# Performance work log

Measured on AMD Instinct MI355X. Metric: run time of the kernel, lower is better.

Reference implementation:

```python
import jax, jax.numpy as jnp
import numpy as np

N_NODES = 100000
N_EDGES = 1600000
NFEAT = 512
HIDDEN = 128
NCLASS = 40


def setup_inputs() -> dict:
    key = jax.random.key(0)
    ks = jax.random.split(key, 8)
    x = jax.random.normal(ks[0], (N_NODES, NFEAT), dtype=jnp.float32)
    edge_src = jax.random.randint(ks[1], (N_EDGES,), 0, N_NODES, dtype=jnp.int32)
    edge_dst = jax.random.randint(ks[2], (N_EDGES,), 0, N_NODES, dtype=jnp.int32)
    # normalized adjacency values (D^-1/2 A D^-1/2 style), all positive
    edge_val = jax.random.uniform(ks[3], (N_EDGES,), dtype=jnp.float32)
    # glorot-ish init like pygcn's reset_parameters
    W1 = jax.random.normal(ks[4], (NFEAT, HIDDEN), dtype=jnp.float32) / np.sqrt(NFEAT)
    b1 = jnp.zeros((HIDDEN,), dtype=jnp.float32)
    W2 = jax.random.normal(ks[5], (HIDDEN, NCLASS), dtype=jnp.float32) / np.sqrt(HIDDEN)
    b2 = jnp.zeros((NCLASS,), dtype=jnp.float32)
    return {"x": x, "edge_src": edge_src, "edge_dst": edge_dst, "edge_val": edge_val,
            "W1": W1, "b1": b1, "W2": W2, "b2": b2}


def _gcn_layer(h, edge_src, edge_dst, edge_val, W, b):
    # support = h @ W ; out = spmm(adj, support) + b
    support = h @ W                                  # [N, d_out]
    msg = support[edge_src] * edge_val[:, None]      # [E, d_out] gather
    agg = jax.ops.segment_sum(msg, edge_dst, num_segments=N_NODES)  # scatter-add
    return agg + b


def reference(x, edge_src, edge_dst, edge_val, W1, b1, W2, b2):
    h = _gcn_layer(x, edge_src, edge_dst, edge_val, W1, b1)
    h = jax.nn.relu(h)
    # dropout=0.0 -> branch skipped (faithful to `if self.dropout:` with falsy value)
    h = _gcn_layer(h, edge_src, edge_dst, edge_val, W2, b2)
    return jax.nn.log_softmax(h, axis=1)
```

## Files before the change

kernel.cpp:

```cpp
#include <hip/hip_runtime.h>
#include <stdint.h>

#define NN 100000
#define NE 1600000
#define NF 512
#define NH 128
#define NC 40
#define NGB 782

typedef float f32x4 __attribute__((ext_vector_type(4)));
typedef short bf16x8 __attribute__((ext_vector_type(8)));

__device__ __forceinline__ unsigned short f2bf(float f){
    unsigned u = __float_as_uint(f);
    u = u + 0x7FFFu + ((u >> 16) & 1u);
    return (unsigned short)(u >> 16);
}
__device__ __forceinline__ unsigned pk2(float a, float b){
    return (unsigned)f2bf(a) | ((unsigned)f2bf(b) << 16);
}
__device__ __forceinline__ float blo(unsigned u){ return __uint_as_float(u << 16); }
__device__ __forceinline__ float bhi(unsigned u){ return __uint_as_float(u & 0xffff0000u); }
__device__ __forceinline__ float pval(unsigned p){ return __uint_as_float((p & 0x7fffu) << 16); }
__device__ __forceinline__ unsigned psrc(unsigned p){ return p >> 15; }

__global__ __launch_bounds__(256) void wprep(const float* __restrict__ W1, const float* __restrict__ W2,
                                             unsigned short* __restrict__ W1t, unsigned short* __restrict__ W2t){
    int tid = blockIdx.x * 256 + threadIdx.x;
    if (tid < NF * NH){
        int c = tid >> 9;
        int k = tid & 511;
        W1t[c * NF + k] = f2bf(W1[k * NH + c]);
    }
    int t2 = tid - NF * NH;
    if (t2 >= 0 && t2 < 48 * NH){
        int c = t2 >> 7;
        int k = t2 & 127;
        W2t[c * NH + k] = (c < NC) ? f2bf(W2[k * NC + c]) : (unsigned short)0;
    }
}

__global__ __launch_bounds__(256, 3) void gemm1_edge(const float* __restrict__ x,
                                                     const unsigned short* __restrict__ W1t,
                                                     unsigned short* __restrict__ s1,
                                                     const int* __restrict__ esrc,
                                                     const int* __restrict__ edst,
                                                     const float* __restrict__ eval,
                                                     unsigned* __restrict__ pkc){
    __shared__ unsigned short Al[2][128 * 40];
    __shared__ unsigned short Bl[2][128 * 40];
    if (blockIdx.x >= NGB){
        int tid = (blockIdx.x - NGB) * 256 + threadIdx.x;
        if (tid < NE){
            int d = edst[tid];
            unsigned pv = ((unsigned)esrc[tid] << 15) | ((unsigned)f2bf(eval[tid]) & 0x7fffu);
            unsigned pos = atomicAdd(&pkc[(size_t)d * 64], 1u);
            if (pos < 63u)
                pkc[(size_t)d * 64 + 1 + pos] = pv;
        }
        return;
    }
    const int tid  = threadIdx.x;
    const int wid  = tid >> 6;
    const int lane = tid & 63;
    const int quad = lane >> 4;
    const int l15  = lane & 15;
    const int br   = blockIdx.x * 128;

    const int r    = tid >> 1;
    const int half = tid & 1;

    int arow = br + r; if (arow >= NN) arow = NN - 1;
    const float* aptr = x + (size_t)arow * NF + half * 16;
    const unsigned short* bptr = W1t + (size_t)r * NF + half * 16;

    float4 pa0, pa1, pa2, pa3;
    uint4  pb0, pb1;
    {
        const float4* ap = (const float4*)aptr;
        pa0 = ap[0]; pa1 = ap[1]; pa2 = ap[2]; pa3 = ap[3];
        const uint4* bp = (const uint4*)bptr;
        pb0 = bp[0]; pb1 = bp[1];
        unsigned* Ad = (unsigned*)&Al[0][r * 40 + half * 16];
        Ad[0] = pk2(pa0.x, pa0.y); Ad[1] = pk2(pa0.z, pa0.w);
        Ad[2] = pk2(pa1.x, pa1.y); Ad[3] = pk2(pa1.z, pa1.w);
        Ad[4] = pk2(pa2.x, pa2.y); Ad[5] = pk2(pa2.z, pa2.w);
        Ad[6] = pk2(pa3.x, pa3.y); Ad[7] = pk2(pa3.z, pa3.w);
        uint4* Bd = (uint4*)&Bl[0][r * 40 + half * 16];
        Bd[0] = pb0; Bd[1] = pb1;
    }
    __syncthreads();

    f32x4 acc[2][8];
#pragma unroll
    for (int i = 0; i < 2; i++)
#pragma unroll
        for (int j = 0; j < 8; j++) acc[i][j] = (f32x4){0.f, 0.f, 0.f, 0.f};

    int cur = 0;
    for (int ks = 0; ks < NF; ks += 32){
        const bool more = (ks + 32 < NF);
        if (more){
            const float4* ap = (const float4*)(aptr + ks + 32);
            pa0 = ap[0]; pa1 = ap[1]; pa2 = ap[2]; pa3 = ap[3];
            const uint4* bp = (const uint4*)(bptr + ks + 32);
            pb0 = bp[0]; pb1 = bp[1];
        }

        bf16x8 a0 = *(const bf16x8*)&Al[cur][(wid * 32 +      l15) * 40 + quad * 8];
        bf16x8 a1 = *(const bf16x8*)&Al[cur][(wid * 32 + 16 + l15) * 40 + quad * 8];
        bf16x8 bb[8];
#pragma unroll
        for (int ct = 0; ct < 8; ct++)
            bb[ct] = *(const bf16x8*)&Bl[cur][(ct * 16 + l15) * 40 + quad * 8];
#pragma unroll
        for (int ct = 0; ct < 8; ct++){
            acc[0][ct] = __builtin_amdgcn_mfma_f32_16x16x32_bf16(a0, bb[ct], acc[0][ct], 0, 0, 0);
            acc[1][ct] = __builtin_amdgcn_mfma_f32_16x16x32_bf16(a1, bb[ct], acc[1][ct], 0, 0, 0);
        }

        if (more){
            int nxt = cur ^ 1;
            unsigned* Ad = (unsigned*)&Al[nxt][r * 40 + half * 16];
            Ad[0] = pk2(pa0.x, pa0.y); Ad[1] = pk2(pa0.z, pa0.w);
            Ad[2] = pk2(pa1.x, pa1.y); Ad[3] = pk2(pa1.z, pa1.w);
            Ad[4] = pk2(pa2.x, pa2.y); Ad[5] = pk2(pa2.z, pa2.w);
            Ad[6] = pk2(pa3.x, pa3.y); Ad[7] = pk2(pa3.z, pa3.w);
            uint4* Bd = (uint4*)&Bl[nxt][r * 40 + half * 16];
            Bd[0] = pb0; Bd[1] = pb1;
        }
        __syncthreads();
        cur ^= 1;
    }

#pragma unroll
    for (int rt = 0; rt < 2; rt++)
#pragma unroll
        for (int ct = 0; ct < 8; ct++)
#pragma unroll
            for (int i = 0; i < 4; i++){
                int row = br + wid * 32 + rt * 16 + quad * 4 + i;
                if (row < NN) s1[(size_t)row * NH + ct * 16 + l15] = f2bf(acc[rt][ct][i]);
            }
}

__global__ __launch_bounds__(256) void agg1g2(const uint4* __restrict__ s1v,
                                              const unsigned* __restrict__ pkc,
                                              const float* __restrict__ b1,
                                              const unsigned short* __restrict__ W2t,
                                              unsigned short* __restrict__ s2p){
    __shared__ unsigned short Hl[64][136];
    const int tid   = threadIdx.x;
    const int wid   = tid >> 6;
    const int lane  = tid & 63;
    const int quad  = lane >> 4;
    const int hl    = lane & 15;
    const int lbase = quad * 16;
    const int nb    = blockIdx.x * 64;

    const float4* b1v = (const float4*)b1;
    const float4 bA = b1v[2 * hl], bB = b1v[2 * hl + 1];

#pragma unroll
    for (int pass = 0; pass < 4; pass++){
        const int nloc = pass * 16 + wid * 4 + quad;
        const int node = nb + nloc;
        float a[8];
#pragma unroll
        for (int t = 0; t < 8; t++) a[t] = 0.f;

        if (node < NN){
            const unsigned sbase = (unsigned)node * 64;
            unsigned rec = pkc[sbase + hl];
            unsigned cntw = __shfl(rec, lbase, 64);
            int dg = (cntw > 63u) ? 63 : (int)cntw;
            int done = 0, lskip = 1;
            unsigned sb = sbase;
            while (done < dg){
                int cnt = dg - done;
                int room = 16 - lskip; if (cnt > room) cnt = room;
                unsigned curc = rec;
                unsigned nsb = sb + 16;
                if (done + cnt < dg) rec = pkc[nsb + hl];
                int j = 0;
                for (; j + 8 <= cnt; j += 8){
                    unsigned ps[8];
#pragma unroll
                    for (int q = 0; q < 8; q++) ps[q] = __shfl(curc, lbase + lskip + j + q, 64);
                    uint4 us[8];
#pragma unroll
                    for (int q = 0; q < 8; q++) us[q] = s1v[(size_t)psrc(ps[q]) * 16 + hl];
#pragma unroll
                    for (int q = 0; q < 8; q++){
                        float v = pval(ps[q]);
                        a[0] += v * blo(us[q].x); a[1] += v * bhi(us[q].x);
                        a[2] += v * blo(us[q].y); a[3] += v * bhi(us[q].y);
                        a[4] += v * blo(us[q].z); a[5] += v * bhi(us[q].z);
                        a[6] += v * blo(us[q].w); a[7] += v * bhi(us[q].w);
                    }
                }
                for (; j + 4 <= cnt; j += 4){
                    unsigned ps[4];
#pragma unroll
                    for (int q = 0; q < 4; q++) ps[q] = __shfl(curc, lbase + lskip + j + q, 64);
                    uint4 us[4];
#pragma unroll
                    for (int q = 0; q < 4; q++) us[q] = s1v[(size_t)psrc(ps[q]) * 16 + hl];
#pragma unroll
                    for (int q = 0; q < 4; q++){
                        float v = pval(ps[q]);
                        a[0] += v * blo(us[q].x); a[1] += v * bhi(us[q].x);
                        a[2] += v * blo(us[q].y); a[3] += v * bhi(us[q].y);
                        a[4] += v * blo(us[q].z); a[5] += v * bhi(us[q].z);
                        a[6] += v * blo(us[q].w); a[7] += v * bhi(us[q].w);
                    }
                }
                for (; j < cnt; j++){
                    unsigned p = __shfl(curc, lbase + lskip + j, 64);
                    float v = pval(p);
                    uint4 u  = s1v[(size_t)psrc(p) * 16 + hl];
                    a[0] += v * blo(u.x); a[1] += v * bhi(u.x);
                    a[2] += v * blo(u.y); a[3] += v * bhi(u.y);
                    a[4] += v * blo(u.z); a[5] += v * bhi(u.z);
                    a[6] += v * blo(u.w); a[7] += v * bhi(u.w);
                }
                done += cnt; sb = nsb; lskip = 0;
            }
            a[0] += bA.x; a[1] += bA.y; a[2] += bA.z; a[3] += bA.w;
            a[4] += bB.x; a[5] += bB.y; a[6] += bB.z; a[7] += bB.w;
#pragma unroll
            for (int t = 0; t < 8; t++) a[t] = fmaxf(a[t], 0.f);
        }
        *(uint4*)&Hl[nloc][hl * 8] = make_uint4(pk2(a[0], a[1]), pk2(a[2], a[3]),
                                                pk2(a[4], a[5]), pk2(a[6], a[7]));
    }
    __syncthreads();

    bf16x8 bf[3][4];
#pragma unroll
    for (int ct = 0; ct < 3; ct++)
#pragma unroll
        for (int ks = 0; ks < 4; ks++)
            bf[ct][ks] = *(const bf16x8*)&W2t[(ct * 16 + hl) * NH + ks * 32 + quad * 8];

    bf16x8 af[4];
#pragma unroll
    for (int ks = 0; ks < 4; ks++)
        af[ks] = *(const bf16x8*)&Hl[wid * 16 + hl][ks * 32 + quad * 8];

    f32x4 acc[3];
#pragma unroll
    for (int ct = 0; ct < 3; ct++) acc[ct] = (f32x4){0.f, 0.f, 0.f, 0.f};
#pragma unroll
    for (int ks = 0; ks < 4; ks++)
#pragma unroll
        for (int ct = 0; ct < 3; ct++)
            acc[ct] = __builtin_amdgcn_mfma_f32_16x16x32_bf16(af[ks], bf[ct][ks], acc[ct], 0, 0, 0);

#pragma unroll
    for (int ct = 0; ct < 3; ct++)
#pragma unroll
        for (int i = 0; i < 4; i++){
            int row = nb + wid * 16 + quad * 4 + i;
            if (row < NN) s2p[(size_t)row * 64 + ct * 16 + hl] = f2bf(acc[ct][i]);
        }
}

__global__ __launch_bounds__(256) void agg2(const uint4* __restrict__ s2v,
                                            const unsigned* __restrict__ pkc,
                                            const float* __restrict__ b2, float* __restrict__ out){
    const int lane  = threadIdx.x & 63;
    const int oct   = lane >> 3;
    const int hl    = lane & 7;
    const int lbase = oct * 8;
    const int node  = blockIdx.x * 32 + (threadIdx.x >> 6) * 8 + oct;

    float a[8];
#pragma unroll
    for (int t = 0; t < 8; t++) a[t] = 0.f;

    const unsigned sbase = (unsigned)node * 64;
    unsigned rec = pkc[sbase + hl];
    unsigned cntw = __shfl(rec, lbase, 64);
    int dg = (cntw > 63u) ? 63 : (int)cntw;
    int done = 0, lskip = 1;
    unsigned sb = sbase;
    while (done < dg){
        int cnt = dg - done;
        int room = 8 - lskip; if (cnt > room) cnt = room;
        unsigned curc = rec;
        unsigned nsb = sb + 8;
        if (done + cnt < dg) rec = pkc[nsb + hl];
        int j = 0;
        for (; j + 4 <= cnt; j += 4){
            unsigned ps[4];
#pragma unroll
            for (int q = 0; q < 4; q++) ps[q] = __shfl(curc, lbase + lskip + j + q, 64);
            uint4 us[4];
#pragma unroll
            for (int q = 0; q < 4; q++) us[q] = s2v[(size_t)psrc(ps[q]) * 8 + hl];
#pragma unroll
            for (int q = 0; q < 4; q++){
                float v = pval(ps[q]);
                a[0] += v * blo(us[q].x); a[1] += v * bhi(us[q].x);
                a[2] += v * blo(us[q].y); a[3] += v * bhi(us[q].y);
                a[4] += v * blo(us[q].z); a[5] += v * bhi(us[q].z);
                a[6] += v * blo(us[q].w); a[7] += v * bhi(us[q].w);
            }
        }
        for (; j < cnt; j++){
            unsigned p = __shfl(curc, lbase + lskip + j, 64);
            float v = pval(p);
            uint4 u  = s2v[(size_t)psrc(p) * 8 + hl];
            a[0] += v * blo(u.x); a[1] += v * bhi(u.x);
            a[2] += v * blo(u.y); a[3] += v * bhi(u.y);
            a[4] += v * blo(u.z); a[5] += v * bhi(u.z);
            a[6] += v * blo(u.w); a[7] += v * bhi(u.w);
        }
        done += cnt; sb = nsb; lskip = 0;
    }
    const bool act = hl < 5;
    float z[8];
    if (act){
        const float4* b2v = (const float4*)b2;
        float4 cA = b2v[2 * hl], cB = b2v[2 * hl + 1];
        z[0] = a[0] + cA.x; z[1] = a[1] + cA.y; z[2] = a[2] + cA.z; z[3] = a[3] + cA.w;
        z[4] = a[4] + cB.x; z[5] = a[5] + cB.y; z[6] = a[6] + cB.z; z[7] = a[7] + cB.w;
    } else {
#pragma unroll
        for (int t = 0; t < 8; t++) z[t] = -INFINITY;
    }
    float m = z[0];
#pragma unroll
    for (int t = 1; t < 8; t++) m = fmaxf(m, z[t]);
#pragma unroll
    for (int o = 4; o; o >>= 1) m = fmaxf(m, __shfl_xor(m, o, 64));
    float pe = 0.f;
    if (act){
#pragma unroll
        for (int t = 0; t < 8; t++) pe += __expf(z[t] - m);
    }
#pragma unroll
    for (int o = 4; o; o >>= 1) pe += __shfl_xor(pe, o, 64);
    if (act){
        float l = __logf(pe) + m;
        float* op = out + (size_t)node * NC + 8 * hl;
        *(float4*)op       = make_float4(z[0] - l, z[1] - l, z[2] - l, z[3] - l);
        *(float4*)(op + 4) = make_float4(z[4] - l, z[5] - l, z[6] - l, z[7] - l);
    }
}

extern "C" void kernel_launch(void* const* d_in, const int* in_sizes, int n_in,
                              void* d_out, int out_size, void* d_ws, size_t ws_size,
                              hipStream_t stream) {
    const float* x    = (const float*)d_in[0];
    const int*   esrc = (const int*)  d_in[1];
    const int*   edst = (const int*)  d_in[2];
    const float* eval = (const float*)d_in[3];
    const float* W1   = (const float*)d_in[4];
    const float* b1   = (const float*)d_in[5];
    const float* W2   = (const float*)d_in[6];
    const float* b2   = (const float*)d_in[7];
    float* out = (float*)d_out;

    char* ws = (char*)d_ws;
    size_t off = 0;
    auto alloc = [&](size_t bytes) -> void* {
        void* p = ws + off;
        off += (bytes + 255) & ~(size_t)255;
        return p;
    };
    unsigned short* W1t  = (unsigned short*)alloc((size_t)NF * NH * 2);
    unsigned short* W2t  = (unsigned short*)alloc((size_t)48 * NH * 2);
    unsigned short* s1   = (unsigned short*)alloc((size_t)NN * NH * 2);
    unsigned short* s2p  = (unsigned short*)alloc((size_t)NN * 64 * 2);
    unsigned*       pkc  = (unsigned*)     alloc((size_t)NN * 64 * 4);

    hipMemsetAsync(pkc, 0, (size_t)NN * 64 * 4, stream);

    wprep     <<<280, 256, 0, stream>>>(W1, W2, W1t, W2t);
    gemm1_edge<<<NGB + (NE + 255) / 256, 256, 0, stream>>>(x, W1t, s1, esrc, edst, eval, pkc);
    agg1g2    <<<(NN + 63) / 64, 256, 0, stream>>>((const uint4*)s1, pkc, b1, W2t, s2p);
    agg2      <<<NN / 32, 256, 0, stream>>>((const uint4*)s2p, pkc, b2, out);
}
```

Baseline: 511.7 us.

## Split degree counters from edge slots and fold edge binning into GEMM blocks

Moves the per-node degree counter out of the packed edge-slot array into a separate padded array, so only that small array is memset instead of the whole 25.6MB slot buffer. Edge binning is now spread over the GEMM blocks: each block loads 8 edges per thread and does the atomics before the GEMM, then writes the packed records after it. This hides the atomic latency behind the matrix work and drops the extra edge-only blocks. The aggregation kernels read the degree from the new array and no longer skip a header slot, and the middle 4-wide unroll path is removed. Costs are extra registers held across the GEMM, which may lower occupancy, and each GEMM block must now cover 2048 edges.

```diff
diff --git a/kernel.cpp b/kernel.cpp
--- a/kernel.cpp
+++ b/kernel.cpp
@@ -6,7 +6,9 @@
 #define NF 512
 #define NH 128
 #define NC 40
+#define DEGS 16
 #define NGB 782
+#define EPB 2048
 
 typedef float f32x4 __attribute__((ext_vector_type(4)));
 typedef short bf16x8 __attribute__((ext_vector_type(8)));
@@ -46,21 +48,28 @@
                                                      const int* __restrict__ esrc,
                                                      const int* __restrict__ edst,
                                                      const float* __restrict__ eval,
+                                                     unsigned* __restrict__ deg,
                                                      unsigned* __restrict__ pkc){
     __shared__ unsigned short Al[2][128 * 40];
     __shared__ unsigned short Bl[2][128 * 40];
-    if (blockIdx.x >= NGB){
-        int tid = (blockIdx.x - NGB) * 256 + threadIdx.x;
-        if (tid < NE){
-            int d = edst[tid];
-            unsigned pv = ((unsigned)esrc[tid] << 15) | ((unsigned)f2bf(eval[tid]) & 0x7fffu);
-            unsigned pos = atomicAdd(&pkc[(size_t)d * 64], 1u);
-            if (pos < 63u)
-                pkc[(size_t)d * 64 + 1 + pos] = pv;
-        }
-        return;
-    }
     const int tid  = threadIdx.x;
+
+    unsigned epv[8]; unsigned epos[8]; int edd[8];
+    {
+        const int ebase = blockIdx.x * EPB + tid;
+#pragma unroll
+        for (int i = 0; i < 8; i++){
+            int e = ebase + i * 256;
+            bool ok = e < NE;
+            int d      = ok ? edst[e] : 0;
+            int sv     = ok ? esrc[e] : 0;
+            float ev   = ok ? eval[e] : 0.f;
+            edd[i] = d;
+            epv[i] = ((unsigned)sv << 15) | ((unsigned)f2bf(ev) & 0x7fffu);
+            epos[i] = ok ? atomicAdd(&deg[d * DEGS], 1u) : 64u;
+        }
+    }
+
     const int wid  = tid >> 6;
     const int lane = tid & 63;
     const int quad = lane >> 4;
@@ -142,9 +151,16 @@
                 int row = br + wid * 32 + rt * 16 + quad * 4 + i;
                 if (row < NN) s1[(size_t)row * NH + ct * 16 + l15] = f2bf(acc[rt][ct][i]);
             }
+
+#pragma unroll
+    for (int i = 0; i < 8; i++){
+        if (epos[i] < 64u)
+            pkc[(size_t)edd[i] * 64 + epos[i]] = epv[i];
+    }
 }
 
 __global__ __launch_bounds__(256) void agg1g2(const uint4* __restrict__ s1v,
+                                              const unsigned* __restrict__ deg,
                                               const unsigned* __restrict__ pkc,
                                               const float* __restrict__ b1,
                                               const unsigned short* __restrict__ W2t,
@@ -170,23 +186,26 @@
         for (int t = 0; t < 8; t++) a[t] = 0.f;
 
         if (node < NN){
-            const unsigned sbase = (unsigned)node * 64;
-            unsigned rec = pkc[sbase + hl];
-            unsigned cntw = __shfl(rec, lbase, 64);
-            int dg = (cntw > 63u) ? 63 : (int)cntw;
-            int done = 0, lskip = 1;
-            unsigned sb = sbase;
-            while (done < dg){
-                int cnt = dg - done;
-                int room = 16 - lskip; if (cnt > room) cnt = room;
+            const unsigned s = (unsigned)node * 64;
+            unsigned dgv = deg[node * DEGS]; int dg = (dgv > 64u) ? 64 : (int)dgv;
+            const unsigned e = s + dg;
+
+            unsigned rec = 0;
+            { int c0 = dg > 16 ? 16 : dg; if (hl < c0) rec = pkc[s + hl]; }
+            for (unsigned base = s; base < e; base += 16){
+                int cnt = (int)(e - base); if (cnt > 16) cnt = 16;
                 unsigned curc = rec;
-                unsigned nsb = sb + 16;
-                if (done + cnt < dg) rec = pkc[nsb + hl];
+                unsigned nxb = base + 16;
+                if (nxb < e){
+                    int cn = (int)(e - nxb); if (cn > 16) cn = 16;
+                    rec = 0;
+                    if (hl < cn) rec = pkc[nxb + hl];
+                }
                 int j = 0;
                 for (; j + 8 <= cnt; j += 8){
                     unsigned ps[8];
 #pragma unroll
-                    for (int q = 0; q < 8; q++) ps[q] = __shfl(curc, lbase + lskip + j + q, 64);
+                    for (int q = 0; q < 8; q++) ps[q] = __shfl(curc, lbase + j + q, 64);
                     uint4 us[8];
 #pragma unroll
                     for (int q = 0; q < 8; q++) us[q] = s1v[(size_t)psrc(ps[q]) * 16 + hl];
@@ -199,24 +218,8 @@
                         a[6] += v * blo(us[q].w); a[7] += v * bhi(us[q].w);
                     }
                 }
-                for (; j + 4 <= cnt; j += 4){
-                    unsigned ps[4];
-#pragma unroll
-                    for (int q = 0; q < 4; q++) ps[q] = __shfl(curc, lbase + lskip + j + q, 64);
-                    uint4 us[4];
-#pragma unroll
-                    for (int q = 0; q < 4; q++) us[q] = s1v[(size_t)psrc(ps[q]) * 16 + hl];
-#pragma unroll
-                    for (int q = 0; q < 4; q++){
-                        float v = pval(ps[q]);
-                        a[0] += v * blo(us[q].x); a[1] += v * bhi(us[q].x);
-                        a[2] += v * blo(us[q].y); a[3] += v * bhi(us[q].y);
-                        a[4] += v * blo(us[q].z); a[5] += v * bhi(us[q].z);
-                        a[6] += v * blo(us[q].w); a[7] += v * bhi(us[q].w);
-                    }
-                }
                 for (; j < cnt; j++){
-                    unsigned p = __shfl(curc, lbase + lskip + j, 64);
+                    unsigned p = __shfl(curc, lbase + j, 64);
                     float v = pval(p);
                     uint4 u  = s1v[(size_t)psrc(p) * 16 + hl];
                     a[0] += v * blo(u.x); a[1] += v * bhi(u.x);
@@ -224,7 +227,6 @@
                     a[4] += v * blo(u.z); a[5] += v * bhi(u.z);
                     a[6] += v * blo(u.w); a[7] += v * bhi(u.w);
                 }
-                done += cnt; sb = nsb; lskip = 0;
             }
             a[0] += bA.x; a[1] += bA.y; a[2] += bA.z; a[3] += bA.w;
             a[4] += bB.x; a[5] += bB.y; a[6] += bB.z; a[7] += bB.w;
@@ -267,6 +269,7 @@
 }
 
 __global__ __launch_bounds__(256) void agg2(const uint4* __restrict__ s2v,
+                                            const unsigned* __restrict__ deg,
                                             const unsigned* __restrict__ pkc,
                                             const float* __restrict__ b2, float* __restrict__ out){
     const int lane  = threadIdx.x & 63;
@@ -279,23 +282,26 @@
 #pragma unroll
     for (int t = 0; t < 8; t++) a[t] = 0.f;
 
-    const unsigned sbase = (unsigned)node * 64;
-    unsigned rec = pkc[sbase + hl];
-    unsigned cntw = __shfl(rec, lbase, 64);
-    int dg = (cntw > 63u) ? 63 : (int)cntw;
-    int done = 0, lskip = 1;
-    unsigned sb = sbase;
-    while (done < dg){
-        int cnt = dg - done;
-        int room = 8 - lskip; if (cnt > room) cnt = room;
+    const unsigned s = (unsigned)node * 64;
+    unsigned dgv = deg[node * DEGS]; int dg = (dgv > 64u) ? 64 : (int)dgv;
+    const unsigned e = s + dg;
+
+    unsigned rec = 0;
+    { int c0 = dg > 8 ? 8 : dg; if (hl < c0) rec = pkc[s + hl]; }
+    for (unsigned base = s; base < e; base += 8){
+        int cnt = (int)(e - base); if (cnt > 8) cnt = 8;
         unsigned curc = rec;
-        unsigned nsb = sb + 8;
-        if (done + cnt < dg) rec = pkc[nsb + hl];
+        unsigned nxb = base + 8;
+        if (nxb < e){
+            int cn = (int)(e - nxb); if (cn > 8) cn = 8;
+            rec = 0;
+            if (hl < cn) rec = pkc[nxb + hl];
+        }
         int j = 0;
         for (; j + 4 <= cnt; j += 4){
             unsigned ps[4];
 #pragma unroll
-            for (int q = 0; q < 4; q++) ps[q] = __shfl(curc, lbase + lskip + j + q, 64);
+            for (int q = 0; q < 4; q++) ps[q] = __shfl(curc, lbase + j + q, 64);
             uint4 us[4];
 #pragma unroll
             for (int q = 0; q < 4; q++) us[q] = s2v[(size_t)psrc(ps[q]) * 8 + hl];
@@ -309,7 +315,7 @@
             }
         }
         for (; j < cnt; j++){
-            unsigned p = __shfl(curc, lbase + lskip + j, 64);
+            unsigned p = __shfl(curc, lbase + j, 64);
             float v = pval(p);
             uint4 u  = s2v[(size_t)psrc(p) * 8 + hl];
             a[0] += v * blo(u.x); a[1] += v * bhi(u.x);
@@ -317,7 +323,6 @@
             a[4] += v * blo(u.z); a[5] += v * bhi(u.z);
             a[6] += v * blo(u.w); a[7] += v * bhi(u.w);
         }
-        done += cnt; sb = nsb; lskip = 0;
     }
     const bool act = hl < 5;
     float z[8];
@@ -374,12 +379,13 @@
     unsigned short* W2t  = (unsigned short*)alloc((size_t)48 * NH * 2);
     unsigned short* s1   = (unsigned short*)alloc((size_t)NN * NH * 2);
     unsigned short* s2p  = (unsigned short*)alloc((size_t)NN * 64 * 2);
+    unsigned*       deg  = (unsigned*)     alloc((size_t)NN * DEGS * 4);
     unsigned*       pkc  = (unsigned*)     alloc((size_t)NN * 64 * 4);
 
-    hipMemsetAsync(pkc, 0, (size_t)NN * 64 * 4, stream);
+    hipMemsetAsync(deg, 0, (size_t)NN * DEGS * 4, stream);
 
     wprep     <<<280, 256, 0, stream>>>(W1, W2, W1t, W2t);
-    gemm1_edge<<<NGB + (NE + 255) / 256, 256, 0, stream>>>(x, W1t, s1, esrc, edst, eval, pkc);
-    agg1g2    <<<(NN + 63) / 64, 256, 0, stream>>>((const uint4*)s1, pkc, b1, W2t, s2p);
-    agg2      <<<NN / 32, 256, 0, stream>>>((const uint4*)s2p, pkc, b2, out);
-}
+    gemm1_edge<<<NGB, 256, 0, stream>>>(x, W1t, s1, esrc, edst, eval, deg, pkc);
+    agg1g2    <<<(NN + 63) / 64, 256, 0, stream>>>((const uint4*)s1, deg, pkc, b1, W2t, s2p);
+    agg2      <<<NN / 32, 256, 0, stream>>>((const uint4*)s2p, deg, pkc, b2, out);
+}
```

Result: slower. 533.0 us (+4.2%).
